# Kernel optimization log

Measured on AMD Instinct MI355X. Metric: run time of the kernel, lower is better.

Reference implementation:

```python
import jax, jax.numpy as jnp
import numpy as np

B, T, V, E, H, C = 128, 200, 50000, 300, 512, 3

def _lstm_scan(x, W_ih, W_hh, b_ih, b_hh, h0, c0):
    # x: [B,T,E]; torch LSTMCell gate order: i, f, g, o
    xg = jnp.einsum('bte,ge->btg', x, W_ih) + b_ih + b_hh  # [B,T,4H]
    def step(carry, xg_t):
        h, c = carry
        gates = xg_t + h @ W_hh.T
        i, f, g, o = jnp.split(gates, 4, axis=-1)
        c = jax.nn.sigmoid(f) * c + jax.nn.sigmoid(i) * jnp.tanh(g)
        h = jax.nn.sigmoid(o) * jnp.tanh(c)
        return (h, c), (h, c)
    _, (hs, cs) = jax.lax.scan(step, (h0, c0), jnp.swapaxes(xg, 0, 1))
    return hs, cs  # [T,B,H]

def _mask_blend(hs, cs, m, h0, c0):
    # hs,cs: [T,B,H]; m: [T,B]; carry-forward previous state where mask==0
    def step(carry, inp):
        h_p, c_p = carry
        h_t, c_t, m_t = inp
        m_t = m_t[:, None]
        h_p = m_t * h_t + (1.0 - m_t) * h_p
        c_p = m_t * c_t + (1.0 - m_t) * c_p
        return (h_p, c_p), (h_p, c_p)
    _, (mh, mc) = jax.lax.scan(step, (h0, c0), (hs, cs, m))
    return mh, mc

def setup_inputs() -> dict:
    key = jax.random.key(0)
    ks = jax.random.split(key, 12)
    s_e = 1.0 / np.sqrt(H)
    u = lambda k, shp: jax.random.uniform(k, shp, jnp.float32, -s_e, s_e)
    return {
        'premise': jax.random.randint(ks[0], (B, T), 0, V),
        'hypothesis': jax.random.randint(ks[1], (B, T), 0, V),
        'similarity': jax.random.uniform(ks[2], (B, 1), jnp.float32),
        'emb_weight': jax.random.normal(ks[3], (V, E), jnp.float32),
        'Wih_p': u(ks[4], (4 * H, E)), 'Whh_p': u(ks[5], (4 * H, H)),
        'bih_p': u(ks[6], (4 * H,)), 'bhh_p': u(ks[7], (4 * H,)),
        'Wih_h': u(ks[8], (4 * H, E)), 'Whh_h': u(ks[9], (4 * H, H)),
        'bih_h': u(ks[10], (4 * H,)), 'bhh_h': u(ks[11], (4 * H,)),
        'fc_W': jax.random.normal(jax.random.fold_in(key, 100), (C, H + 1), jnp.float32) * 0.02,
        'fc_b': jnp.zeros((C,), jnp.float32),
    }

def reference(premise, hypothesis, similarity, emb_weight,
              Wih_p, Whh_p, bih_p, bhh_p, Wih_h, Whh_h, bih_h, bhh_h,
              fc_W, fc_b):
    emb_p = emb_weight[premise]            # [B,T,E]
    emb_h = emb_weight[hypothesis]
    mask_p = (premise != 0).astype(jnp.float32).T   # [T,B]
    mask_h = (hypothesis != 0).astype(jnp.float32).T
    h0 = jnp.zeros((B, H), jnp.float32)
    c0 = jnp.zeros((B, H), jnp.float32)
    # premise LSTM (raw, unmasked recurrence as in original)
    hs_p, cs_p = _lstm_scan(emb_p, Wih_p, Whh_p, bih_p, bhh_p, h0, c0)
    _, mc_p = _mask_blend(hs_p, cs_p, mask_p, h0, c0)
    c_last = mc_p[-1]                      # masked last premise cell
    # hypothesis LSTM: hidden reset, cell carried
    hs_h, cs_h = _lstm_scan(emb_h, Wih_h, Whh_h, bih_h, bhh_h, h0, c_last)
    mh_h, _ = _mask_blend(hs_h, cs_h, mask_h, h0, c_last)
    feat = jnp.concatenate([mh_h[-1], similarity], axis=1)  # [B,H+1]
    logits = feat @ fc_W.T + fc_b
    # dropout inactive (eval mode)
    return jax.nn.log_softmax(logits, axis=1)
```

## Files before the change

### kernel.cpp

```cpp
#include <hip/hip_runtime.h>
#include <hip/hip_bf16.h>

#define B_ 128
#define T_ 200
#define H_ 512
#define G_ 2048
#define E_ 300

typedef unsigned short u16;
typedef unsigned int u32;

using f32x4 = __attribute__((ext_vector_type(4))) float;
using s16x8 = __attribute__((ext_vector_type(8))) short;
using u32x2 = __attribute__((ext_vector_type(2))) u32;

__device__ __forceinline__ u16 f2bf(float f) {
  u32 u = __builtin_bit_cast(u32, f);
  u32 r = (u + 0x7fffu + ((u >> 16) & 1u)) >> 16;
  return (u16)r;
}
__device__ __forceinline__ float bf2f(u16 s) {
  return __builtin_bit_cast(float, (u32)s << 16);
}

__device__ __forceinline__ s16x8 ld_h16_sc(const void* p) {
  s16x8 r;
  asm volatile("global_load_dwordx4 %0, %1, off sc0 sc1" : "=v"(r) : "v"(p));
  return r;
}
__device__ __forceinline__ void st_h_sc(void* p, u32 v) {
  asm volatile("global_store_short %0, %1, off sc0 sc1" :: "v"(p), "v"(v));
}
__device__ __forceinline__ u32 ld_flag_sc(const void* p) {
  u32 r;
  asm volatile("global_load_dword %0, %1, off sc0 sc1\n\ts_waitcnt vmcnt(0)"
               : "=v"(r) : "v"(p) : "memory");
  return r;
}
__device__ __forceinline__ void st_flag_sc(void* p, u32 v) {
  asm volatile("global_store_dword %0, %1, off sc0 sc1" :: "v"(p), "v"(v) : "memory");
}

__global__ __launch_bounds__(256) void wih_cvt(
    const float* __restrict__ W, u16* __restrict__ Wb)
{
  const int idx = blockIdx.x * 256 + threadIdx.x;
  const int row = idx / 320, k = idx - row * 320;
  const float v = (k < E_) ? W[row * E_ + k] : 0.f;
  Wb[idx] = f2bf(v);
}

__global__ __launch_bounds__(64) void mask_k(
    const int* __restrict__ tok, u32* __restrict__ mb)
{
  const int idx = blockIdx.x * 64 + threadIdx.x;
  if (idx >= T_ * 4) return;
  const int t = idx >> 2, w = idx & 3;
  u32 bits = 0;
  for (int i = 0; i < 32; ++i)
    bits |= (tok[(w * 32 + i) * T_ + t] != 0 ? 1u : 0u) << i;
  mb[idx] = bits;
}

__global__ __launch_bounds__(256) void xg_gemm(
    const int* __restrict__ tok, const float* __restrict__ emb,
    const u16* __restrict__ Wb, const float* __restrict__ bih,
    const float* __restrict__ bhh, u16* __restrict__ xg)
{
  __shared__ u16 Al[64 * 320];
  __shared__ u16 Bl[32 * 320];
  __shared__ int tks[64];
  const int tid = threadIdx.x;
  const int bx = blockIdx.x;
  const int m0 = bx * 64;
  if (tid < 64) tks[tid] = tok[((bx & 1) * 64 + tid) * T_ + (bx >> 1)];
  __syncthreads();
  {
    const int row = tid >> 2, part = tid & 3;
    const float* erow = emb + (size_t)tks[row] * E_;
    char* base = (char*)Al + row * 640;
    const int swz = (row & 7) << 4;
#pragma unroll
    for (int i = 0; i < 40; ++i) {
      const int kw = part * 40 + i;
      const int k = kw * 2;
      const float v0 = (k < E_) ? erow[k] : 0.f;
      const float v1 = (k + 1 < E_) ? erow[k + 1] : 0.f;
      *(u32*)(base + ((kw * 4) ^ swz)) = (u32)f2bf(v0) | ((u32)f2bf(v1) << 16);
    }
  }
  __syncthreads();
  const int wv = tid >> 6, ln = tid & 63, lr = ln & 15, lq = ln >> 4;
  const int arow = wv * 16 + lr;
  const char* abase = (const char*)Al + arow * 640;
  const int aswz = (arow & 7) << 4;
  const int brow = tid >> 3, bpart = tid & 7;
  char* bdst = (char*)Bl + brow * 640;
  const int bswz = (brow & 7) << 4;
  const char* b0base = (const char*)Bl + lr * 640;
  const char* b1base = (const char*)Bl + (16 + lr) * 640;
  const int bswz2 = (lr & 7) << 4;

  for (int ni = 0; ni < 8; ++ni) {
    const int n0 = blockIdx.y * 256 + ni * 32;
    {
      const u16* src = Wb + (size_t)(n0 + brow) * 320 + bpart * 40;
#pragma unroll
      for (int i = 0; i < 5; ++i) {
        s16x8 v = *(const s16x8*)(src + i * 8);
        *(s16x8*)(bdst + (((bpart * 5 + i) * 16) ^ bswz)) = v;
      }
    }
    __syncthreads();
    f32x4 acc0 = {0.f, 0.f, 0.f, 0.f}, acc1 = {0.f, 0.f, 0.f, 0.f};
#pragma unroll
    for (int ks = 0; ks < 10; ++ks) {
      const int kb = ks * 64 + lq * 16;
      s16x8 af  = *(const s16x8*)(abase  + (kb ^ aswz));
      s16x8 bf0 = *(const s16x8*)(b0base + (kb ^ bswz2));
      s16x8 bf1 = *(const s16x8*)(b1base + (kb ^ bswz2));
      acc0 = __builtin_amdgcn_mfma_f32_16x16x32_bf16(af, bf0, acc0, 0, 0, 0);
      acc1 = __builtin_amdgcn_mfma_f32_16x16x32_bf16(af, bf1, acc1, 0, 0, 0);
    }
    const int qc = n0 >> 9;
    const int jA = (n0 & 511) + lr;
#pragma unroll
    for (int r = 0; r < 4; ++r) {
      const int m = m0 + wv * 16 + lq * 4 + r;
      const int gA = n0 + lr, gB = n0 + 16 + lr;
      xg[(size_t)m * 2048 + (size_t)jA * 4 + qc]        = f2bf(acc0[r] + bih[gA] + bhh[gA]);
      xg[(size_t)m * 2048 + (size_t)(jA + 16) * 4 + qc] = f2bf(acc1[r] + bih[gB] + bhh[gB]);
    }
    __syncthreads();
  }
}

template<int TRACK_C>
__global__ __launch_bounds__(512, 2) void lstm_rec(
    const u16* __restrict__ xg, const float* __restrict__ Whh,
    u16* __restrict__ hbuf, const float* __restrict__ c0in,
    float* __restrict__ cOut, float* __restrict__ mhOut,
    u32* __restrict__ flags, const u32* __restrict__ maskb)
{
  __shared__ f32x4 red[8][4][64];
  const int tid = threadIdx.x;
  const int wv = tid >> 6, ln = tid & 63, lr = ln & 15, lq = ln >> 4;
  const int grp = (int)blockIdx.x >> 5, jt = (int)blockIdx.x & 31;
  const int j0 = jt * 16, bg0 = grp * 16;
  u32* gflags = flags + grp * 512;

  s16x8 Bf[4][2];
#pragma unroll
  for (int q = 0; q < 4; ++q) {
    const float* wr = Whh + (size_t)(q * H_ + j0 + lr) * H_ + wv * 64 + lq * 8;
#pragma unroll
    for (int ks = 0; ks < 2; ++ks) {
      const float* wp = wr + ks * 32;
      s16x8 f;
#pragma unroll
      for (int i = 0; i < 8; ++i) f[i] = (short)f2bf(wp[i]);
      Bf[q][ks] = f;
    }
  }

  float c[4], mb[4];
#pragma unroll
  for (int r = 0; r < 4; ++r) {
    const int b = bg0 + lq * 4 + r;
    float cv = 0.f;
    if (!TRACK_C && wv == 0) cv = c0in[b * H_ + j0 + lr];
    c[r] = cv;
    mb[r] = TRACK_C ? cv : 0.f;
  }

  const u32* pp = gflags + (ln & 31) * 16;
  const int mword = grp >> 1, mshift = (grp & 1) * 16;

  for (int t = 0; t < T_; ++t) {
    const u16* hrd = hbuf + (t & 1) * (B_ * H_);
    u16* hwr = hbuf + ((t + 1) & 1) * (B_ * H_);

    u32x2 gxp[4];
    u32 mku = 0;
    if (wv == 0) {
      mku = maskb[t * 4 + mword] >> mshift;
#pragma unroll
      for (int r = 0; r < 4; ++r) {
        const int b = bg0 + lq * 4 + r;
        gxp[r] = *(const u32x2*)(xg + (size_t)(t * 128 + b) * 2048
                                    + (size_t)(j0 + lr) * 4);
      }
      if (t > 0) {
        int guard = 0;
        for (;;) {
          u32 v = ld_flag_sc(pp);
          if (__all((int)(v >= (u32)t))) break;
          if (++guard > (1 << 22)) break;
          __builtin_amdgcn_s_sleep(1);
        }
      }
    }
    __syncthreads();
    __builtin_amdgcn_sched_barrier(0);

    s16x8 ha0, ha1;
    const u16* hb = hrd + (size_t)(bg0 + lr) * H_ + wv * 64 + lq * 8;
    ha0 = ld_h16_sc(hb);
    ha1 = ld_h16_sc(hb + 32);
    asm volatile("s_waitcnt vmcnt(0)" ::: "memory");
    __builtin_amdgcn_sched_barrier(0);

    f32x4 acc[4];
#pragma unroll
    for (int q = 0; q < 4; ++q) {
      acc[q] = __builtin_amdgcn_mfma_f32_16x16x32_bf16(ha0, Bf[q][0],
                   (f32x4){0.f, 0.f, 0.f, 0.f}, 0, 0, 0);
      acc[q] = __builtin_amdgcn_mfma_f32_16x16x32_bf16(ha1, Bf[q][1], acc[q], 0, 0, 0);
    }

    if (wv > 0) {
#pragma unroll
      for (int q = 0; q < 4; ++q) red[wv][q][ln] = acc[q];
    }
    __syncthreads();
    if (wv == 0) {
#pragma unroll
      for (int kv = 1; kv < 8; ++kv)
#pragma unroll
        for (int q = 0; q < 4; ++q) acc[q] += red[kv][q][ln];
      const bool last = (t == T_ - 1);
#pragma unroll
      for (int r = 0; r < 4; ++r) {
        const int b = bg0 + lq * 4 + r;
        const u32 lo = gxp[r][0], hi = gxp[r][1];
        const float gi = acc[0][r] + bf2f((u16)lo);
        const float gf = acc[1][r] + bf2f((u16)(lo >> 16));
        const float gG = acc[2][r] + bf2f((u16)hi);
        const float go = acc[3][r] + bf2f((u16)(hi >> 16));
        const float si = 1.f / (1.f + __expf(-gi));
        const float sf = 1.f / (1.f + __expf(-gf));
        const float so = 1.f / (1.f + __expf(-go));
        const float tg = 2.f / (1.f + __expf(-2.f * gG)) - 1.f;
        const float cn = sf * c[r] + si * tg;
        const float tc = 2.f / (1.f + __expf(-2.f * cn)) - 1.f;
        const float hn = so * tc;
        c[r] = cn;
        if ((mku >> (lq * 4 + r)) & 1u) mb[r] = TRACK_C ? cn : hn;
        if (!last) st_h_sc(hwr + (size_t)b * H_ + j0 + lr, (u32)f2bf(hn));
      }
      if (t + 1 < T_) {
        asm volatile("s_waitcnt vmcnt(0)" ::: "memory");
        if (ln == 0) st_flag_sc(gflags + jt * 16, (u32)(t + 1));
      }
    }
  }

  if (wv == 0) {
#pragma unroll
    for (int r = 0; r < 4; ++r) {
      const int b = bg0 + lq * 4 + r;
      if (TRACK_C) cOut[b * H_ + j0 + lr] = mb[r];
      else         mhOut[b * H_ + j0 + lr] = mb[r];
    }
  }
}

__global__ __launch_bounds__(128) void final_k(
    const float* __restrict__ mh, const float* __restrict__ sim,
    const float* __restrict__ fcW, const float* __restrict__ fcb,
    float* __restrict__ out)
{
  const int b = threadIdx.x;
  float l[3];
#pragma unroll
  for (int cc = 0; cc < 3; ++cc) {
    const float* wr = fcW + cc * (H_ + 1);
    float s = fcb[cc] + sim[b] * wr[H_];
    for (int j = 0; j < H_; ++j) s += mh[b * H_ + j] * wr[j];
    l[cc] = s;
  }
  const float m = fmaxf(l[0], fmaxf(l[1], l[2]));
  const float lse = m + logf(__expf(l[0] - m) + __expf(l[1] - m) + __expf(l[2] - m));
  out[b * 3 + 0] = l[0] - lse;
  out[b * 3 + 1] = l[1] - lse;
  out[b * 3 + 2] = l[2] - lse;
}

extern "C" void kernel_launch(void* const* d_in, const int* in_sizes, int n_in,
                              void* d_out, int out_size, void* d_ws, size_t ws_size,
                              hipStream_t stream) {
  const int*   prem = (const int*)d_in[0];
  const int*   hypo = (const int*)d_in[1];
  const float* sim  = (const float*)d_in[2];
  const float* emb  = (const float*)d_in[3];
  const float* WihP = (const float*)d_in[4];
  const float* WhhP = (const float*)d_in[5];
  const float* bihP = (const float*)d_in[6];
  const float* bhhP = (const float*)d_in[7];
  const float* WihH = (const float*)d_in[8];
  const float* WhhH = (const float*)d_in[9];
  const float* bihH = (const float*)d_in[10];
  const float* bhhH = (const float*)d_in[11];
  const float* fcW  = (const float*)d_in[12];
  const float* fcb  = (const float*)d_in[13];
  float* out = (float*)d_out;

  char* ws = (char*)d_ws;
  const size_t XG_BYTES = (size_t)B_ * T_ * G_ * 2;
  const size_t HB_OFF = XG_BYTES;
  const size_t CL_OFF = HB_OFF + (size_t)2 * B_ * H_ * 2;
  const size_t MH_OFF = CL_OFF + (size_t)B_ * H_ * 4;
  const size_t FL_OFF = MH_OFF + (size_t)B_ * H_ * 4;
  const size_t MK_OFF = FL_OFF + 32768;
  const size_t WB_OFF = MK_OFF + 8192;
  const size_t NEED   = WB_OFF + (size_t)G_ * 320 * 2;
  if (ws_size < NEED) return;

  u16*   xg    = (u16*)ws;
  u16*   hbuf  = (u16*)(ws + HB_OFF);
  float* cLast = (float*)(ws + CL_OFF);
  float* mh    = (float*)(ws + MH_OFF);
  u32*   flagsP = (u32*)(ws + FL_OFF);
  u32*   flagsH = flagsP + 4096;
  u32*   maskbP = (u32*)(ws + MK_OFF);
  u32*   maskbH = maskbP + 1024;
  u16*   Wb    = (u16*)(ws + WB_OFF);

  hipMemsetAsync(ws + FL_OFF, 0, 32768, stream);

  dim3 gG(400, 8);
  wih_cvt<<<2560, 256, 0, stream>>>(WihP, Wb);
  mask_k<<<13, 64, 0, stream>>>(prem, maskbP);
  xg_gemm<<<gG, 256, 0, stream>>>(prem, emb, Wb, bihP, bhhP, xg);
  hipMemsetAsync(hbuf, 0, (size_t)B_ * H_ * 2, stream);
  lstm_rec<1><<<256, 512, 0, stream>>>(xg, WhhP, hbuf, nullptr, cLast, nullptr, flagsP, maskbP);
  wih_cvt<<<2560, 256, 0, stream>>>(WihH, Wb);
  mask_k<<<13, 64, 0, stream>>>(hypo, maskbH);
  xg_gemm<<<gG, 256, 0, stream>>>(hypo, emb, Wb, bihH, bhhH, xg);
  hipMemsetAsync(hbuf, 0, (size_t)B_ * H_ * 2, stream);
  lstm_rec<0><<<256, 512, 0, stream>>>(xg, WhhH, hbuf, cLast, nullptr, mh, flagsH, maskbH);
  final_k<<<1, 128, 0, stream>>>(mh, sim, fcW, fcb, out);
}
```

Before: 2.034 ms.

## Fuse input-projection GEMM into recurrent LSTM kernel, computed one step ahead

Removes the separate weight conversion and xg GEMM kernels along with the large bf16 xg workspace. Inside the recurrent kernel, waves 4-7 keep the W_ih slices in registers and compute the next timestep's input projection with MFMA while wave 0 polls flags, double-buffering the result in shared memory. The biases are added in registers. This cuts launches and HBM traffic for xg, but adds register pressure, a per-step embedding gather on the critical loop, and an extra __syncthreads per step.

```diff
diff --git a/kernel.cpp b/kernel.cpp
--- a/kernel.cpp
+++ b/kernel.cpp
@@ -12,7 +12,6 @@
 
 using f32x4 = __attribute__((ext_vector_type(4))) float;
 using s16x8 = __attribute__((ext_vector_type(8))) short;
-using u32x2 = __attribute__((ext_vector_type(2))) u32;
 
 __device__ __forceinline__ u16 f2bf(float f) {
   u32 u = __builtin_bit_cast(u32, f);
@@ -39,15 +38,6 @@
 }
 __device__ __forceinline__ void st_flag_sc(void* p, u32 v) {
   asm volatile("global_store_dword %0, %1, off sc0 sc1" :: "v"(p), "v"(v) : "memory");
-}
-
-__global__ __launch_bounds__(256) void wih_cvt(
-    const float* __restrict__ W, u16* __restrict__ Wb)
-{
-  const int idx = blockIdx.x * 256 + threadIdx.x;
-  const int row = idx / 320, k = idx - row * 320;
-  const float v = (k < E_) ? W[row * E_ + k] : 0.f;
-  Wb[idx] = f2bf(v);
 }
 
 __global__ __launch_bounds__(64) void mask_k(
@@ -62,87 +52,17 @@
   mb[idx] = bits;
 }
 
-__global__ __launch_bounds__(256) void xg_gemm(
-    const int* __restrict__ tok, const float* __restrict__ emb,
-    const u16* __restrict__ Wb, const float* __restrict__ bih,
-    const float* __restrict__ bhh, u16* __restrict__ xg)
-{
-  __shared__ u16 Al[64 * 320];
-  __shared__ u16 Bl[32 * 320];
-  __shared__ int tks[64];
-  const int tid = threadIdx.x;
-  const int bx = blockIdx.x;
-  const int m0 = bx * 64;
-  if (tid < 64) tks[tid] = tok[((bx & 1) * 64 + tid) * T_ + (bx >> 1)];
-  __syncthreads();
-  {
-    const int row = tid >> 2, part = tid & 3;
-    const float* erow = emb + (size_t)tks[row] * E_;
-    char* base = (char*)Al + row * 640;
-    const int swz = (row & 7) << 4;
-#pragma unroll
-    for (int i = 0; i < 40; ++i) {
-      const int kw = part * 40 + i;
-      const int k = kw * 2;
-      const float v0 = (k < E_) ? erow[k] : 0.f;
-      const float v1 = (k + 1 < E_) ? erow[k + 1] : 0.f;
-      *(u32*)(base + ((kw * 4) ^ swz)) = (u32)f2bf(v0) | ((u32)f2bf(v1) << 16);
-    }
-  }
-  __syncthreads();
-  const int wv = tid >> 6, ln = tid & 63, lr = ln & 15, lq = ln >> 4;
-  const int arow = wv * 16 + lr;
-  const char* abase = (const char*)Al + arow * 640;
-  const int aswz = (arow & 7) << 4;
-  const int brow = tid >> 3, bpart = tid & 7;
-  char* bdst = (char*)Bl + brow * 640;
-  const int bswz = (brow & 7) << 4;
-  const char* b0base = (const char*)Bl + lr * 640;
-  const char* b1base = (const char*)Bl + (16 + lr) * 640;
-  const int bswz2 = (lr & 7) << 4;
-
-  for (int ni = 0; ni < 8; ++ni) {
-    const int n0 = blockIdx.y * 256 + ni * 32;
-    {
-      const u16* src = Wb + (size_t)(n0 + brow) * 320 + bpart * 40;
-#pragma unroll
-      for (int i = 0; i < 5; ++i) {
-        s16x8 v = *(const s16x8*)(src + i * 8);
-        *(s16x8*)(bdst + (((bpart * 5 + i) * 16) ^ bswz)) = v;
-      }
-    }
-    __syncthreads();
-    f32x4 acc0 = {0.f, 0.f, 0.f, 0.f}, acc1 = {0.f, 0.f, 0.f, 0.f};
-#pragma unroll
-    for (int ks = 0; ks < 10; ++ks) {
-      const int kb = ks * 64 + lq * 16;
-      s16x8 af  = *(const s16x8*)(abase  + (kb ^ aswz));
-      s16x8 bf0 = *(const s16x8*)(b0base + (kb ^ bswz2));
-      s16x8 bf1 = *(const s16x8*)(b1base + (kb ^ bswz2));
-      acc0 = __builtin_amdgcn_mfma_f32_16x16x32_bf16(af, bf0, acc0, 0, 0, 0);
-      acc1 = __builtin_amdgcn_mfma_f32_16x16x32_bf16(af, bf1, acc1, 0, 0, 0);
-    }
-    const int qc = n0 >> 9;
-    const int jA = (n0 & 511) + lr;
-#pragma unroll
-    for (int r = 0; r < 4; ++r) {
-      const int m = m0 + wv * 16 + lq * 4 + r;
-      const int gA = n0 + lr, gB = n0 + 16 + lr;
-      xg[(size_t)m * 2048 + (size_t)jA * 4 + qc]        = f2bf(acc0[r] + bih[gA] + bhh[gA]);
-      xg[(size_t)m * 2048 + (size_t)(jA + 16) * 4 + qc] = f2bf(acc1[r] + bih[gB] + bhh[gB]);
-    }
-    __syncthreads();
-  }
-}
-
 template<int TRACK_C>
 __global__ __launch_bounds__(512, 2) void lstm_rec(
-    const u16* __restrict__ xg, const float* __restrict__ Whh,
+    const int* __restrict__ tok, const float* __restrict__ emb,
+    const float* __restrict__ Wih, const float* __restrict__ bih,
+    const float* __restrict__ bhh, const float* __restrict__ Whh,
     u16* __restrict__ hbuf, const float* __restrict__ c0in,
     float* __restrict__ cOut, float* __restrict__ mhOut,
     u32* __restrict__ flags, const u32* __restrict__ maskb)
 {
   __shared__ f32x4 red[8][4][64];
+  __shared__ f32x4 xr[2][4][64];
   const int tid = threadIdx.x;
   const int wv = tid >> 6, ln = tid & 63, lr = ln & 15, lq = ln >> 4;
   const int grp = (int)blockIdx.x >> 5, jt = (int)blockIdx.x & 31;
@@ -163,7 +83,23 @@
     }
   }
 
-  float c[4], mb[4];
+  const int qq = wv - 4;
+  s16x8 Wf[10];
+  if (wv >= 4) {
+    const float* wr = Wih + (size_t)(qq * H_ + j0 + lr) * E_;
+#pragma unroll
+    for (int ks = 0; ks < 10; ++ks) {
+      s16x8 f;
+#pragma unroll
+      for (int i = 0; i < 8; ++i) {
+        const int k = ks * 32 + lq * 8 + i;
+        f[i] = (short)((k < E_) ? f2bf(wr[k]) : (u16)0);
+      }
+      Wf[ks] = f;
+    }
+  }
+
+  float c[4], mb[4], bias[4];
 #pragma unroll
   for (int r = 0; r < 4; ++r) {
     const int b = bg0 + lq * 4 + r;
@@ -172,6 +108,31 @@
     c[r] = cv;
     mb[r] = TRACK_C ? cv : 0.f;
   }
+  if (wv == 0) {
+#pragma unroll
+    for (int q = 0; q < 4; ++q) {
+      const int g = q * H_ + j0 + lr;
+      bias[q] = bih[g] + bhh[g];
+    }
+  }
+
+  if (wv >= 4) {
+    const int tk = tok[(bg0 + lr) * T_ + 0];
+    const float* er = emb + (size_t)tk * E_;
+    f32x4 xacc = {0.f, 0.f, 0.f, 0.f};
+#pragma unroll
+    for (int ks = 0; ks < 10; ++ks) {
+      s16x8 af;
+#pragma unroll
+      for (int i = 0; i < 8; ++i) {
+        const int k = ks * 32 + lq * 8 + i;
+        af[i] = (short)((k < E_) ? f2bf(er[k]) : (u16)0);
+      }
+      xacc = __builtin_amdgcn_mfma_f32_16x16x32_bf16(af, Wf[ks], xacc, 0, 0, 0);
+    }
+    xr[0][qq][ln] = xacc;
+  }
+  __syncthreads();
 
   const u32* pp = gflags + (ln & 31) * 16;
   const int mword = grp >> 1, mshift = (grp & 1) * 16;
@@ -180,16 +141,9 @@
     const u16* hrd = hbuf + (t & 1) * (B_ * H_);
     u16* hwr = hbuf + ((t + 1) & 1) * (B_ * H_);
 
-    u32x2 gxp[4];
     u32 mku = 0;
     if (wv == 0) {
       mku = maskb[t * 4 + mword] >> mshift;
-#pragma unroll
-      for (int r = 0; r < 4; ++r) {
-        const int b = bg0 + lq * 4 + r;
-        gxp[r] = *(const u32x2*)(xg + (size_t)(t * 128 + b) * 2048
-                                    + (size_t)(j0 + lr) * 4);
-      }
       if (t > 0) {
         int guard = 0;
         for (;;) {
@@ -199,6 +153,21 @@
           __builtin_amdgcn_s_sleep(1);
         }
       }
+    } else if (wv >= 4 && t + 1 < T_) {
+      const int tk = tok[(bg0 + lr) * T_ + (t + 1)];
+      const float* er = emb + (size_t)tk * E_;
+      f32x4 xacc = {0.f, 0.f, 0.f, 0.f};
+#pragma unroll
+      for (int ks = 0; ks < 10; ++ks) {
+        s16x8 af;
+#pragma unroll
+        for (int i = 0; i < 8; ++i) {
+          const int k = ks * 32 + lq * 8 + i;
+          af[i] = (short)((k < E_) ? f2bf(er[k]) : (u16)0);
+        }
+        xacc = __builtin_amdgcn_mfma_f32_16x16x32_bf16(af, Wf[ks], xacc, 0, 0, 0);
+      }
+      xr[(t + 1) & 1][qq][ln] = xacc;
     }
     __syncthreads();
     __builtin_amdgcn_sched_barrier(0);
@@ -228,15 +197,17 @@
       for (int kv = 1; kv < 8; ++kv)
 #pragma unroll
         for (int q = 0; q < 4; ++q) acc[q] += red[kv][q][ln];
+      f32x4 xv[4];
+#pragma unroll
+      for (int q = 0; q < 4; ++q) xv[q] = xr[t & 1][q][ln];
       const bool last = (t == T_ - 1);
 #pragma unroll
       for (int r = 0; r < 4; ++r) {
         const int b = bg0 + lq * 4 + r;
-        const u32 lo = gxp[r][0], hi = gxp[r][1];
-        const float gi = acc[0][r] + bf2f((u16)lo);
-        const float gf = acc[1][r] + bf2f((u16)(lo >> 16));
-        const float gG = acc[2][r] + bf2f((u16)hi);
-        const float go = acc[3][r] + bf2f((u16)(hi >> 16));
+        const float gi = acc[0][r] + xv[0][r] + bias[0];
+        const float gf = acc[1][r] + xv[1][r] + bias[1];
+        const float gG = acc[2][r] + xv[2][r] + bias[2];
+        const float go = acc[3][r] + xv[3][r] + bias[3];
         const float si = 1.f / (1.f + __expf(-gi));
         const float sf = 1.f / (1.f + __expf(-gf));
         const float so = 1.f / (1.f + __expf(-go));
@@ -253,6 +224,7 @@
         if (ln == 0) st_flag_sc(gflags + jt * 16, (u32)(t + 1));
       }
     }
+    __syncthreads();
   }
 
   if (wv == 0) {
@@ -306,17 +278,14 @@
   float* out = (float*)d_out;
 
   char* ws = (char*)d_ws;
-  const size_t XG_BYTES = (size_t)B_ * T_ * G_ * 2;
-  const size_t HB_OFF = XG_BYTES;
+  const size_t HB_OFF = 0;
   const size_t CL_OFF = HB_OFF + (size_t)2 * B_ * H_ * 2;
   const size_t MH_OFF = CL_OFF + (size_t)B_ * H_ * 4;
   const size_t FL_OFF = MH_OFF + (size_t)B_ * H_ * 4;
   const size_t MK_OFF = FL_OFF + 32768;
-  const size_t WB_OFF = MK_OFF + 8192;
-  const size_t NEED   = WB_OFF + (size_t)G_ * 320 * 2;
+  const size_t NEED   = MK_OFF + 8192;
   if (ws_size < NEED) return;
 
-  u16*   xg    = (u16*)ws;
   u16*   hbuf  = (u16*)(ws + HB_OFF);
   float* cLast = (float*)(ws + CL_OFF);
   float* mh    = (float*)(ws + MH_OFF);
@@ -324,20 +293,18 @@
   u32*   flagsH = flagsP + 4096;
   u32*   maskbP = (u32*)(ws + MK_OFF);
   u32*   maskbH = maskbP + 1024;
-  u16*   Wb    = (u16*)(ws + WB_OFF);
 
   hipMemsetAsync(ws + FL_OFF, 0, 32768, stream);
 
-  dim3 gG(400, 8);
-  wih_cvt<<<2560, 256, 0, stream>>>(WihP, Wb);
   mask_k<<<13, 64, 0, stream>>>(prem, maskbP);
-  xg_gemm<<<gG, 256, 0, stream>>>(prem, emb, Wb, bihP, bhhP, xg);
+  mask_k<<<13, 64, 0, stream>>>(hypo, maskbH);
   hipMemsetAsync(hbuf, 0, (size_t)B_ * H_ * 2, stream);
-  lstm_rec<1><<<256, 512, 0, stream>>>(xg, WhhP, hbuf, nullptr, cLast, nullptr, flagsP, maskbP);
-  wih_cvt<<<2560, 256, 0, stream>>>(WihH, Wb);
-  mask_k<<<13, 64, 0, stream>>>(hypo, maskbH);
-  xg_gemm<<<gG, 256, 0, stream>>>(hypo, emb, Wb, bihH, bhhH, xg);
+  lstm_rec<1><<<256, 512, 0, stream>>>(prem, emb, WihP, bihP, bhhP, WhhP,
+                                       hbuf, nullptr, cLast, nullptr,
+                                       flagsP, maskbP);
   hipMemsetAsync(hbuf, 0, (size_t)B_ * H_ * 2, stream);
-  lstm_rec<0><<<256, 512, 0, stream>>>(xg, WhhH, hbuf, cLast, nullptr, mh, flagsH, maskbH);
+  lstm_rec<0><<<256, 512, 0, stream>>>(hypo, emb, WihH, bihH, bhhH, WhhH,
+                                       hbuf, cLast, nullptr, mh,
+                                       flagsH, maskbH);
   final_k<<<1, 128, 0, stream>>>(mh, sim, fcW, fcb, out);
 }
```

Result: no change. 2.058 ms (+1.2%).
